# Kernel tuning notes

Hardware: AMD Instinct MI355X
Metric: run time of the kernel (lower is better)

## Reference

```python
import jax, jax.numpy as jnp
import numpy as np

NI = 256        # in_channels
QK = NI // 8    # query/key channels = 32
BS, H, W = 4, 64, 64


def setup_inputs() -> dict:
    key = jax.random.key(0)
    ks = jax.random.split(key, 8)
    x = jax.random.normal(ks[0], (BS, NI, H, W), dtype=jnp.float32)
    # 1x1 conv weights stored as [out_ch, in_ch] (kernel is 1x1)
    wq = jax.random.normal(ks[1], (QK, NI), dtype=jnp.float32) * (1.0 / np.sqrt(NI))
    bq = jnp.zeros((QK,), dtype=jnp.float32)
    wk = jax.random.normal(ks[2], (QK, NI), dtype=jnp.float32) * (1.0 / np.sqrt(NI))
    bk = jnp.zeros((QK,), dtype=jnp.float32)
    wv = jax.random.normal(ks[3], (NI, NI), dtype=jnp.float32) * (1.0 / np.sqrt(NI))
    bv = jnp.zeros((NI,), dtype=jnp.float32)
    # gamma is zero-init in the module; use small random values so the
    # attention branch actually contributes (post-training state).
    gamma = jax.random.normal(ks[4], (1, NI, 1, 1), dtype=jnp.float32) * 0.1
    return {"x": x, "wq": wq, "bq": bq, "wk": wk, "bk": bk,
            "wv": wv, "bv": bv, "gamma": gamma}


def reference(x, wq, bq, wk, bk, wv, bv, gamma):
    bs, c, h, w = x.shape
    n = h * w
    xf = x.reshape(bs, c, n)                       # [bs, c, N]
    # 1x1 convs == per-pixel linear maps over channels
    q = jnp.einsum('oc,bcn->bno', wq, xf) + bq     # [bs, N, qk]
    k = jnp.einsum('oc,bcn->bon', wk, xf) + bk[None, :, None]  # [bs, qk, N]
    v = jnp.einsum('oc,bcn->bon', wv, xf) + bv[None, :, None]  # [bs, c, N]
    attn = jax.nn.softmax(jnp.einsum('bnq,bqm->bnm', q, k), axis=-1)  # [bs, N, N]
    out = jnp.einsum('bcm,bnm->bcn', v, attn)      # value @ attn^T
    out = out.reshape(bs, c, h, w)
    return gamma * out + x
```

## Files before the change

### kernel.cpp

```cpp
#include <hip/hip_runtime.h>
#include <cstdint>
#include <cstddef>

#define NI   256
#define QKC  32
#define BS   4
#define NPIX 4096

typedef __bf16 bf16x8 __attribute__((ext_vector_type(8)));
typedef __bf16 bf16x4 __attribute__((ext_vector_type(4)));
typedef float  f32x16 __attribute__((ext_vector_type(16)));

__device__ inline f32x16 zero16() {
    f32x16 z;
    #pragma unroll
    for (int i = 0; i < 16; ++i) z[i] = 0.f;
    return z;
}

__global__ __launch_bounds__(256) void wconv(
    const float* __restrict__ wq, const float* __restrict__ wk,
    const float* __restrict__ wv, __bf16* __restrict__ wbf)
{
    int f = (blockIdx.x * 256 + threadIdx.x) * 4;
    int row = f >> 8, c = f & 255;
    const float* src = row < 32 ? wq + row * NI + c
                     : row < 64 ? wk + (row - 32) * NI + c
                                : wv + (row - 64) * NI + c;
    float4 v = *(const float4*)src;
    __align__(8) __bf16 o4[4] = {(__bf16)v.x, (__bf16)v.y, (__bf16)v.z, (__bf16)v.w};
    *(uint2*)(wbf + f) = *(const uint2*)o4;
}

__global__ __launch_bounds__(256) void qkv_mfma(
    const float* __restrict__ x, const __bf16* __restrict__ wbf,
    const float* __restrict__ bq, const float* __restrict__ bk,
    const float* __restrict__ bv,
    __bf16* __restrict__ qth, __bf16* __restrict__ qtl,
    __bf16* __restrict__ kth, __bf16* __restrict__ vb)
{
    __shared__ __align__(16) __bf16 Wl[160][72];
    __shared__ __align__(16) __bf16 xT[64][72];
    __shared__ float bls[160];

    const int t = threadIdx.x, w = t >> 6, lane = t & 63;
    const int l31 = lane & 31, h = lane >> 5;
    const int b = blockIdx.z, hb = blockIdx.y, n0 = blockIdx.x * 64;

    if (t < 160) {
        int och = hb * 160 + t;
        bls[t] = och < 32 ? bq[och] : och < 64 ? bk[och - 32] : bv[och - 64];
    }

    f32x16 acc[3] = {zero16(), zero16(), zero16()};

    for (int kc = 0; kc < 4; ++kc) {
        __syncthreads();
        #pragma unroll
        for (int i = 0; i < 5; ++i) {
            int e = t + 256 * i; int row = e >> 3, ch = e & 7;
            *(uint4*)&Wl[row][ch * 8] =
                *(const uint4*)(wbf + ((size_t)(hb * 160 + row)) * NI + kc * 64 + ch * 8);
        }
        {
            int n4 = (t & 15) * 4, c4 = (t >> 4) * 4;
            float4 xv[4];
            #pragma unroll
            for (int j = 0; j < 4; ++j)
                xv[j] = *(const float4*)(x + ((size_t)(b * NI) + kc * 64 + c4 + j) * NPIX + n0 + n4);
            #pragma unroll
            for (int i = 0; i < 4; ++i) {
                __align__(8) __bf16 r4[4] = {
                    (__bf16)((&xv[0].x)[i]), (__bf16)((&xv[1].x)[i]),
                    (__bf16)((&xv[2].x)[i]), (__bf16)((&xv[3].x)[i])};
                *(uint2*)&xT[n4 + i][c4] = *(const uint2*)r4;
            }
        }
        __syncthreads();

        #pragma unroll
        for (int kk = 0; kk < 4; ++kk) {
            bf16x8 xf0 = *(const bf16x8*)&xT[l31][kk * 16 + 8 * h];
            bf16x8 xf1 = *(const bf16x8*)&xT[32 + l31][kk * 16 + 8 * h];
            #pragma unroll
            for (int jj = 0; jj < 3; ++jj) {
                int j = w + 4 * jj;
                if (j < 10) {
                    int nt = j & 1, otl = j >> 1;
                    bf16x8 wf = *(const bf16x8*)&Wl[otl * 32 + l31][kk * 16 + 8 * h];
                    bf16x8 xf = nt ? xf1 : xf0;
                    if (hb == 0 && otl < 2)
                        acc[jj] = __builtin_amdgcn_mfma_f32_32x32x16_bf16(xf, wf, acc[jj], 0, 0, 0);
                    else
                        acc[jj] = __builtin_amdgcn_mfma_f32_32x32x16_bf16(wf, xf, acc[jj], 0, 0, 0);
                }
            }
        }
    }

    #pragma unroll
    for (int jj = 0; jj < 3; ++jj) {
        int j = w + 4 * jj;
        if (j >= 10) continue;
        int nt = j & 1, otl = j >> 1;
        int gt = hb * 5 + otl;
        const f32x16& A = acc[jj];
        if (gt < 2) {
            __bf16* dh = gt == 0 ? qth : kth;
            float bias = bls[otl * 32 + l31];
            #pragma unroll
            for (int r = 0; r < 16; ++r) {
                int rit = (r & 3) + 8 * (r >> 2) + 4 * h;
                int n = n0 + nt * 32 + rit;
                float val = A[r] + bias;
                __bf16 hh = (__bf16)val;
                size_t idx = ((size_t)b * NPIX + n) * QKC + l31;
                dh[idx] = hh;
                if (gt == 0) qtl[idx] = (__bf16)(val - (float)hh);
            }
        } else {
            #pragma unroll
            for (int r = 0; r < 16; ++r) {
                int rit = (r & 3) + 8 * (r >> 2) + 4 * h;
                int loc = otl * 32 + rit;
                int c = hb * 160 + loc - 64;
                float val = A[r] + bls[loc];
                vb[((size_t)(b * NI) + c) * NPIX + n0 + nt * 32 + l31] = (__bf16)val;
            }
        }
    }
}

__global__ __launch_bounds__(256) void attn_mfma(
    const __bf16* __restrict__ qth, const __bf16* __restrict__ qtl,
    const __bf16* __restrict__ kth, const __bf16* __restrict__ vb,
    __bf16* __restrict__ Opart, float* __restrict__ dpart)
{
    __shared__ __align__(16) __bf16 pt_s[64][72];
    __shared__ float dbuf[4][36];

    const int t    = threadIdx.x;
    const int b    = blockIdx.z;
    const int ksp  = blockIdx.y;
    const int n0   = blockIdx.x * 64;
    const int w    = t >> 6;
    const int lane = t & 63;
    const int l31  = lane & 31;
    const int h    = lane >> 5;
    const int sr   = w & 1, sc = w >> 1;
    const int mbase = ksp * (NPIX / 2);

    const size_t qrow = ((size_t)b * NPIX + n0 + 32 * sr + l31) * QKC;
    bf16x8 qh0 = *(const bf16x8*)(qth + qrow + 8 * h);
    bf16x8 qh1 = *(const bf16x8*)(qth + qrow + 16 + 8 * h);
    bf16x8 ql0 = *(const bf16x8*)(qtl + qrow + 8 * h);
    bf16x8 ql1 = *(const bf16x8*)(qtl + qrow + 16 + 8 * h);

    const __bf16* kbase  = kth + ((size_t)b * NPIX + mbase + 32 * sc + l31) * QKC + 8 * h;
    const __bf16* vbase0 = vb + ((size_t)(b * NI) + 64 * w + l31) * NPIX + mbase + 8 * h;
    const __bf16* vbase1 = vbase0 + (size_t)32 * NPIX;

    bf16x8 ones;
    #pragma unroll
    for (int i = 0; i < 8; ++i) ones[i] = (__bf16)1.0f;

    f32x16 a00 = zero16(), a01 = zero16(), a10 = zero16(), a11 = zero16();
    f32x16 d = zero16();

    const int NIT = NPIX / 2 / 64;
    bf16x8 kh0 = *(const bf16x8*)kbase;
    bf16x8 kh1 = *(const bf16x8*)(kbase + 16);

    for (int mt = 0; mt < NIT; ++mt) {
        f32x16 s = zero16();
        s = __builtin_amdgcn_mfma_f32_32x32x16_bf16(qh0, kh0, s, 0, 0, 0);
        s = __builtin_amdgcn_mfma_f32_32x32x16_bf16(qh1, kh1, s, 0, 0, 0);
        s = __builtin_amdgcn_mfma_f32_32x32x16_bf16(ql0, kh0, s, 0, 0, 0);
        s = __builtin_amdgcn_mfma_f32_32x32x16_bf16(ql1, kh1, s, 0, 0, 0);

        if (mt < NIT - 1) {
            const __bf16* kp = kbase + (size_t)(mt + 1) * 64 * QKC;
            kh0 = *(const bf16x8*)kp;
            kh1 = *(const bf16x8*)(kp + 16);
        }
        bf16x8 vf0[4], vf1[4];
        #pragma unroll
        for (int ks = 0; ks < 4; ++ks) {
            vf0[ks] = *(const bf16x8*)(vbase0 + (size_t)mt * 64 + ks * 16);
            vf1[ks] = *(const bf16x8*)(vbase1 + (size_t)mt * 64 + ks * 16);
        }

        #pragma unroll
        for (int r = 0; r < 16; ++r) {
            int rit = (r & 3) + 8 * (r >> 2) + 4 * h;
            pt_s[32 * sr + rit][32 * sc + l31] = (__bf16)__expf(s[r]);
        }
        __syncthreads();

        #pragma unroll
        for (int ks = 0; ks < 4; ++ks) {
            bf16x8 pa0 = *(const bf16x8*)&pt_s[l31][ks * 16 + 8 * h];
            bf16x8 pa1 = *(const bf16x8*)&pt_s[32 + l31][ks * 16 + 8 * h];
            if ((ks >> 1) == sc)
                d = __builtin_amdgcn_mfma_f32_32x32x16_bf16(sr ? pa1 : pa0, ones, d, 0, 0, 0);
            a00 = __builtin_amdgcn_mfma_f32_32x32x16_bf16(pa0, vf0[ks], a00, 0, 0, 0);
            a10 = __builtin_amdgcn_mfma_f32_32x32x16_bf16(pa1, vf0[ks], a10, 0, 0, 0);
            a01 = __builtin_amdgcn_mfma_f32_32x32x16_bf16(pa0, vf1[ks], a01, 0, 0, 0);
            a11 = __builtin_amdgcn_mfma_f32_32x32x16_bf16(pa1, vf1[ks], a11, 0, 0, 0);
        }
        __syncthreads();
    }

    if (l31 == 0) {
        #pragma unroll
        for (int r = 0; r < 16; ++r) {
            int rit = (r & 3) + 8 * (r >> 2) + 4 * h;
            dbuf[w][rit] = d[r];
        }
    }
    __syncthreads();
    if (w < 2 && l31 == 0) {
        size_t dbase = ((size_t)(ksp * BS + b)) * NPIX + n0 + 32 * w;
        #pragma unroll
        for (int r = 0; r < 16; ++r) {
            int rit = (r & 3) + 8 * (r >> 2) + 4 * h;
            dpart[dbase + rit] = dbuf[w][rit] + dbuf[w + 2][rit];
        }
    }

    size_t obase = (((size_t)(ksp * BS + b)) * NI + 64 * w + l31) * NPIX + n0;
    #pragma unroll
    for (int rq = 0; rq < 4; ++rq) {
        int nn = 8 * rq + 4 * h;
        __align__(8) __bf16 t00[4], t10[4], t01[4], t11[4];
        #pragma unroll
        for (int i = 0; i < 4; ++i) {
            t00[i] = (__bf16)a00[4 * rq + i];
            t10[i] = (__bf16)a10[4 * rq + i];
            t01[i] = (__bf16)a01[4 * rq + i];
            t11[i] = (__bf16)a11[4 * rq + i];
        }
        *(uint2*)(Opart + obase + nn)                       = *(const uint2*)t00;
        *(uint2*)(Opart + obase + 32 + nn)                  = *(const uint2*)t10;
        *(uint2*)(Opart + obase + (size_t)32 * NPIX + nn)      = *(const uint2*)t01;
        *(uint2*)(Opart + obase + (size_t)32 * NPIX + 32 + nn) = *(const uint2*)t11;
    }
}

__global__ __launch_bounds__(256) void combine(
    const float* __restrict__ x, const float* __restrict__ gamma,
    const __bf16* __restrict__ Opart, const float* __restrict__ dpart,
    float* __restrict__ out)
{
    int idx = (blockIdx.x * 256 + threadIdx.x) * 4;
    int n = idx & (NPIX - 1);
    int c = (idx >> 12) & (NI - 1);
    int b = idx >> 20;

    size_t o0 = (((size_t)(0 * BS + b)) * NI + c) * NPIX + n;
    size_t o1 = (((size_t)(1 * BS + b)) * NI + c) * NPIX + n;
    bf16x4 p0 = *(const bf16x4*)(Opart + o0);
    bf16x4 p1 = *(const bf16x4*)(Opart + o1);
    float4 da = *(const float4*)(dpart + ((size_t)(0 * BS + b)) * NPIX + n);
    float4 db = *(const float4*)(dpart + ((size_t)(1 * BS + b)) * NPIX + n);
    size_t xb = ((size_t)(b * NI) + c) * NPIX + n;
    float4 xv = *(const float4*)(x + xb);
    float g = gamma[c];

    float4 r;
    r.x = g * (((float)p0[0] + (float)p1[0]) / (da.x + db.x)) + xv.x;
    r.y = g * (((float)p0[1] + (float)p1[1]) / (da.y + db.y)) + xv.y;
    r.z = g * (((float)p0[2] + (float)p1[2]) / (da.z + db.z)) + xv.z;
    r.w = g * (((float)p0[3] + (float)p1[3]) / (da.w + db.w)) + xv.w;
    *(float4*)(out + xb) = r;
}

extern "C" void kernel_launch(void* const* d_in, const int* in_sizes, int n_in,
                              void* d_out, int out_size, void* d_ws, size_t ws_size,
                              hipStream_t stream)
{
    const float* x     = (const float*)d_in[0];
    const float* wq    = (const float*)d_in[1];
    const float* bq    = (const float*)d_in[2];
    const float* wk    = (const float*)d_in[3];
    const float* bk    = (const float*)d_in[4];
    const float* wv    = (const float*)d_in[5];
    const float* bv    = (const float*)d_in[6];
    const float* gamma = (const float*)d_in[7];
    float* out = (float*)d_out;

    const size_t WSZ = (size_t)320 * NI;
    const size_t QSZ = (size_t)BS * NPIX * QKC;
    const size_t VSZ = (size_t)BS * NI * NPIX;
    __bf16* wbf   = (__bf16*)d_ws;
    __bf16* qth   = wbf + WSZ;
    __bf16* qtl   = qth + QSZ;
    __bf16* kth   = qtl + QSZ;
    __bf16* vb    = kth + QSZ;
    __bf16* Opart = vb + VSZ;
    float*  dpart = (float*)(Opart + 2 * VSZ);

    wconv<<<dim3(80), 256, 0, stream>>>(wq, wk, wv, wbf);
    qkv_mfma<<<dim3(64, 2, BS), 256, 0, stream>>>(x, wbf, bq, bk, bv,
                                                  qth, qtl, kth, vb);
    attn_mfma<<<dim3(64, 2, BS), 256, 0, stream>>>(qth, qtl, kth, vb, Opart, dpart);
    combine<<<dim3(BS * NI * NPIX / 1024), 256, 0, stream>>>(x, gamma, Opart, dpart, out);
}
```

Baseline: 172.9 us.

## Double-buffer attention P tile and restructure QKV projection per 32-pixel tile

The attention kernel now keeps two P tiles in shared memory and computes the next tile's scores and exponentials before the current tile's PV MFMAs. This removes one barrier per iteration and overlaps exp/LDS writes with matrix work. Q is pre-scaled by log2(e) so the kernel can use the hardware exp2 instruction. The QKV projection is rewritten so each block covers 32 pixels across all 320 output channels: x is staged once in LDS and weights are read straight from global memory instead of through LDS chunks. The trade-off is more LDS use in attention and more global weight traffic in the projection.

After: 181.0 us. +4.7%, slower.

```diff
diff --git a/kernel.cpp b/kernel.cpp
--- a/kernel.cpp
+++ b/kernel.cpp
@@ -39,93 +39,75 @@
     __bf16* __restrict__ qth, __bf16* __restrict__ qtl,
     __bf16* __restrict__ kth, __bf16* __restrict__ vb)
 {
-    __shared__ __align__(16) __bf16 Wl[160][72];
-    __shared__ __align__(16) __bf16 xT[64][72];
-    __shared__ float bls[160];
+    __shared__ __align__(16) __bf16 xT[32][264];
+    __shared__ float bls[320];
 
     const int t = threadIdx.x, w = t >> 6, lane = t & 63;
     const int l31 = lane & 31, h = lane >> 5;
-    const int b = blockIdx.z, hb = blockIdx.y, n0 = blockIdx.x * 64;
-
-    if (t < 160) {
-        int och = hb * 160 + t;
-        bls[t] = och < 32 ? bq[och] : och < 64 ? bk[och - 32] : bv[och - 64];
-    }
+    const int b = blockIdx.y, n0 = blockIdx.x * 32;
+
+    for (int i = t; i < 320; i += 256)
+        bls[i] = i < 32 ? bq[i] : i < 64 ? bk[i - 32] : bv[i - 64];
+
+    {
+        int n4 = (t & 7) * 4, cb = (t >> 3) * 8;
+        float4 xv[8];
+        #pragma unroll
+        for (int j = 0; j < 8; ++j)
+            xv[j] = *(const float4*)(x + ((size_t)(b * NI) + cb + j) * NPIX + n0 + n4);
+        #pragma unroll
+        for (int i = 0; i < 4; ++i) {
+            __align__(16) __bf16 r8[8];
+            #pragma unroll
+            for (int j = 0; j < 8; ++j) r8[j] = (__bf16)((&xv[j].x)[i]);
+            *(uint4*)&xT[n4 + i][cb] = *(const uint4*)r8;
+        }
+    }
+    __syncthreads();
 
     f32x16 acc[3] = {zero16(), zero16(), zero16()};
 
-    for (int kc = 0; kc < 4; ++kc) {
-        __syncthreads();
-        #pragma unroll
-        for (int i = 0; i < 5; ++i) {
-            int e = t + 256 * i; int row = e >> 3, ch = e & 7;
-            *(uint4*)&Wl[row][ch * 8] =
-                *(const uint4*)(wbf + ((size_t)(hb * 160 + row)) * NI + kc * 64 + ch * 8);
-        }
-        {
-            int n4 = (t & 15) * 4, c4 = (t >> 4) * 4;
-            float4 xv[4];
-            #pragma unroll
-            for (int j = 0; j < 4; ++j)
-                xv[j] = *(const float4*)(x + ((size_t)(b * NI) + kc * 64 + c4 + j) * NPIX + n0 + n4);
-            #pragma unroll
-            for (int i = 0; i < 4; ++i) {
-                __align__(8) __bf16 r4[4] = {
-                    (__bf16)((&xv[0].x)[i]), (__bf16)((&xv[1].x)[i]),
-                    (__bf16)((&xv[2].x)[i]), (__bf16)((&xv[3].x)[i])};
-                *(uint2*)&xT[n4 + i][c4] = *(const uint2*)r4;
-            }
-        }
-        __syncthreads();
-
-        #pragma unroll
-        for (int kk = 0; kk < 4; ++kk) {
-            bf16x8 xf0 = *(const bf16x8*)&xT[l31][kk * 16 + 8 * h];
-            bf16x8 xf1 = *(const bf16x8*)&xT[32 + l31][kk * 16 + 8 * h];
-            #pragma unroll
-            for (int jj = 0; jj < 3; ++jj) {
-                int j = w + 4 * jj;
-                if (j < 10) {
-                    int nt = j & 1, otl = j >> 1;
-                    bf16x8 wf = *(const bf16x8*)&Wl[otl * 32 + l31][kk * 16 + 8 * h];
-                    bf16x8 xf = nt ? xf1 : xf0;
-                    if (hb == 0 && otl < 2)
-                        acc[jj] = __builtin_amdgcn_mfma_f32_32x32x16_bf16(xf, wf, acc[jj], 0, 0, 0);
-                    else
-                        acc[jj] = __builtin_amdgcn_mfma_f32_32x32x16_bf16(wf, xf, acc[jj], 0, 0, 0);
-                }
+    #pragma unroll 4
+    for (int kk = 0; kk < 16; ++kk) {
+        bf16x8 xf = *(const bf16x8*)&xT[l31][kk * 16 + 8 * h];
+        #pragma unroll
+        for (int jj = 0; jj < 3; ++jj) {
+            int otl = w + 4 * jj;
+            if (otl < 10) {
+                bf16x8 wf = *(const bf16x8*)(wbf + (size_t)(otl * 32 + l31) * NI + kk * 16 + 8 * h);
+                if (otl < 2)
+                    acc[jj] = __builtin_amdgcn_mfma_f32_32x32x16_bf16(xf, wf, acc[jj], 0, 0, 0);
+                else
+                    acc[jj] = __builtin_amdgcn_mfma_f32_32x32x16_bf16(wf, xf, acc[jj], 0, 0, 0);
             }
         }
     }
 
     #pragma unroll
     for (int jj = 0; jj < 3; ++jj) {
-        int j = w + 4 * jj;
-        if (j >= 10) continue;
-        int nt = j & 1, otl = j >> 1;
-        int gt = hb * 5 + otl;
+        int otl = w + 4 * jj;
+        if (otl >= 10) continue;
         const f32x16& A = acc[jj];
-        if (gt < 2) {
-            __bf16* dh = gt == 0 ? qth : kth;
+        if (otl < 2) {
+            __bf16* dh = otl == 0 ? qth : kth;
             float bias = bls[otl * 32 + l31];
+            float scale = otl == 0 ? 1.4426950408889634f : 1.0f;
             #pragma unroll
             for (int r = 0; r < 16; ++r) {
                 int rit = (r & 3) + 8 * (r >> 2) + 4 * h;
-                int n = n0 + nt * 32 + rit;
-                float val = A[r] + bias;
+                float val = (A[r] + bias) * scale;
                 __bf16 hh = (__bf16)val;
-                size_t idx = ((size_t)b * NPIX + n) * QKC + l31;
+                size_t idx = ((size_t)b * NPIX + n0 + rit) * QKC + l31;
                 dh[idx] = hh;
-                if (gt == 0) qtl[idx] = (__bf16)(val - (float)hh);
+                if (otl == 0) qtl[idx] = (__bf16)(val - (float)hh);
             }
         } else {
             #pragma unroll
             for (int r = 0; r < 16; ++r) {
                 int rit = (r & 3) + 8 * (r >> 2) + 4 * h;
-                int loc = otl * 32 + rit;
-                int c = hb * 160 + loc - 64;
-                float val = A[r] + bls[loc];
-                vb[((size_t)(b * NI) + c) * NPIX + n0 + nt * 32 + l31] = (__bf16)val;
+                int c = otl * 32 + rit - 64;
+                float val = A[r] + bls[otl * 32 + rit];
+                vb[((size_t)(b * NI) + c) * NPIX + n0 + l31] = (__bf16)val;
             }
         }
     }
@@ -136,7 +118,7 @@
     const __bf16* __restrict__ kth, const __bf16* __restrict__ vb,
     __bf16* __restrict__ Opart, float* __restrict__ dpart)
 {
-    __shared__ __align__(16) __bf16 pt_s[64][72];
+    __shared__ __align__(16) __bf16 pt_s[2][64][72];
     __shared__ float dbuf[4][36];
 
     const int t    = threadIdx.x;
@@ -168,21 +150,28 @@
     f32x16 d = zero16();
 
     const int NIT = NPIX / 2 / 64;
+
     bf16x8 kh0 = *(const bf16x8*)kbase;
     bf16x8 kh1 = *(const bf16x8*)(kbase + 16);
-
-    for (int mt = 0; mt < NIT; ++mt) {
+    {
         f32x16 s = zero16();
         s = __builtin_amdgcn_mfma_f32_32x32x16_bf16(qh0, kh0, s, 0, 0, 0);
         s = __builtin_amdgcn_mfma_f32_32x32x16_bf16(qh1, kh1, s, 0, 0, 0);
         s = __builtin_amdgcn_mfma_f32_32x32x16_bf16(ql0, kh0, s, 0, 0, 0);
         s = __builtin_amdgcn_mfma_f32_32x32x16_bf16(ql1, kh1, s, 0, 0, 0);
-
-        if (mt < NIT - 1) {
-            const __bf16* kp = kbase + (size_t)(mt + 1) * 64 * QKC;
-            kh0 = *(const bf16x8*)kp;
-            kh1 = *(const bf16x8*)(kp + 16);
-        }
+        #pragma unroll
+        for (int r = 0; r < 16; ++r) {
+            int rit = (r & 3) + 8 * (r >> 2) + 4 * h;
+            pt_s[0][32 * sr + rit][32 * sc + l31] = (__bf16)__builtin_amdgcn_exp2f(s[r]);
+        }
+    }
+    kh0 = *(const bf16x8*)(kbase + (size_t)64 * QKC);
+    kh1 = *(const bf16x8*)(kbase + (size_t)64 * QKC + 16);
+    __syncthreads();
+
+    for (int mt = 0; mt < NIT; ++mt) {
+        const int cur = mt & 1;
+
         bf16x8 vf0[4], vf1[4];
         #pragma unroll
         for (int ks = 0; ks < 4; ++ks) {
@@ -190,17 +179,28 @@
             vf1[ks] = *(const bf16x8*)(vbase1 + (size_t)mt * 64 + ks * 16);
         }
 
-        #pragma unroll
-        for (int r = 0; r < 16; ++r) {
-            int rit = (r & 3) + 8 * (r >> 2) + 4 * h;
-            pt_s[32 * sr + rit][32 * sc + l31] = (__bf16)__expf(s[r]);
-        }
-        __syncthreads();
+        if (mt < NIT - 1) {
+            f32x16 s = zero16();
+            s = __builtin_amdgcn_mfma_f32_32x32x16_bf16(qh0, kh0, s, 0, 0, 0);
+            s = __builtin_amdgcn_mfma_f32_32x32x16_bf16(qh1, kh1, s, 0, 0, 0);
+            s = __builtin_amdgcn_mfma_f32_32x32x16_bf16(ql0, kh0, s, 0, 0, 0);
+            s = __builtin_amdgcn_mfma_f32_32x32x16_bf16(ql1, kh1, s, 0, 0, 0);
+            if (mt < NIT - 2) {
+                const __bf16* kp = kbase + (size_t)(mt + 2) * 64 * QKC;
+                kh0 = *(const bf16x8*)kp;
+                kh1 = *(const bf16x8*)(kp + 16);
+            }
+            #pragma unroll
+            for (int r = 0; r < 16; ++r) {
+                int rit = (r & 3) + 8 * (r >> 2) + 4 * h;
+                pt_s[1 - cur][32 * sr + rit][32 * sc + l31] = (__bf16)__builtin_amdgcn_exp2f(s[r]);
+            }
+        }
 
         #pragma unroll
         for (int ks = 0; ks < 4; ++ks) {
-            bf16x8 pa0 = *(const bf16x8*)&pt_s[l31][ks * 16 + 8 * h];
-            bf16x8 pa1 = *(const bf16x8*)&pt_s[32 + l31][ks * 16 + 8 * h];
+            bf16x8 pa0 = *(const bf16x8*)&pt_s[cur][l31][ks * 16 + 8 * h];
+            bf16x8 pa1 = *(const bf16x8*)&pt_s[cur][32 + l31][ks * 16 + 8 * h];
             if ((ks >> 1) == sc)
                 d = __builtin_amdgcn_mfma_f32_32x32x16_bf16(sr ? pa1 : pa0, ones, d, 0, 0, 0);
             a00 = __builtin_amdgcn_mfma_f32_32x32x16_bf16(pa0, vf0[ks], a00, 0, 0, 0);
@@ -240,8 +240,8 @@
             t01[i] = (__bf16)a01[4 * rq + i];
             t11[i] = (__bf16)a11[4 * rq + i];
         }
-        *(uint2*)(Opart + obase + nn)                       = *(const uint2*)t00;
-        *(uint2*)(Opart + obase + 32 + nn)                  = *(const uint2*)t10;
+        *(uint2*)(Opart + obase + nn)                          = *(const uint2*)t00;
+        *(uint2*)(Opart + obase + 32 + nn)                     = *(const uint2*)t10;
         *(uint2*)(Opart + obase + (size_t)32 * NPIX + nn)      = *(const uint2*)t01;
         *(uint2*)(Opart + obase + (size_t)32 * NPIX + 32 + nn) = *(const uint2*)t11;
     }
@@ -301,8 +301,8 @@
     float*  dpart = (float*)(Opart + 2 * VSZ);
 
     wconv<<<dim3(80), 256, 0, stream>>>(wq, wk, wv, wbf);
-    qkv_mfma<<<dim3(64, 2, BS), 256, 0, stream>>>(x, wbf, bq, bk, bv,
-                                                  qth, qtl, kth, vb);
+    qkv_mfma<<<dim3(NPIX / 32, BS), 256, 0, stream>>>(x, wbf, bq, bk, bv,
+                                                      qth, qtl, kth, vb);
     attn_mfma<<<dim3(64, 2, BS), 256, 0, stream>>>(qth, qtl, kth, vb, Opart, dpart);
     combine<<<dim3(BS * NI * NPIX / 1024), 256, 0, stream>>>(x, gamma, Opart, dpart, out);
 }
```
